# Kernel tuning notes

Hardware: AMD Instinct MI355X
Metric: run time of the kernel (lower is better)

The kernel has to match this reference:

```python
import jax, jax.numpy as jnp
import numpy as np

N = 100000   # num_labels
E = 3200000  # num edges
F_IN, H1, H2 = 384, 128, 64


def setup_inputs() -> dict:
    key = jax.random.key(0)
    k0, k1, k2, k3 = jax.random.split(key, 4)
    x = jax.random.normal(k0, (N, F_IN), dtype=jnp.float32) * 0.05
    W1 = jax.random.normal(k1, (F_IN, H1), dtype=jnp.float32) * (1.0 / np.sqrt(F_IN))
    b1 = jnp.zeros((H1,), dtype=jnp.float32)
    W2 = jax.random.normal(k2, (H1, H2), dtype=jnp.float32) * (1.0 / np.sqrt(H1))
    b2 = jnp.zeros((H2,), dtype=jnp.float32)
    edge_index = jax.random.randint(k3, (2, E), 0, N, dtype=jnp.int32)
    return {"x": x, "W1": W1, "b1": b1, "W2": W2, "b2": b2, "edge_index": edge_index}


def _gcn_norm(edge_index, num_nodes):
    # PyG gcn_norm: add self loops, deg from dst with unit weights, sym norm.
    loops = jnp.arange(num_nodes, dtype=edge_index.dtype)
    src = jnp.concatenate([edge_index[0], loops])
    dst = jnp.concatenate([edge_index[1], loops])
    deg = jax.ops.segment_sum(jnp.ones_like(dst, dtype=jnp.float32), dst,
                              num_segments=num_nodes)
    dis = jnp.where(deg > 0, jax.lax.rsqrt(deg), 0.0)
    norm = dis[src] * dis[dst]  # [E + N]
    return src, dst, norm


def _gcn_conv(x, W, b, src, dst, norm, num_nodes):
    h = x @ W                                   # [N, out]
    msg = h[src] * norm[:, None]                # gather + scale
    out = jax.ops.segment_sum(msg, dst, num_segments=num_nodes)
    return out + b


def reference(x, W1, b1, W2, b2, edge_index):
    src, dst, norm = _gcn_norm(edge_index, N)
    h = jax.nn.relu(_gcn_conv(x, W1, b1, src, dst, norm, N))
    out = _gcn_conv(h, W2, b2, src, dst, norm, N)
    return out
```

## Files before the change

kernel.cpp:

```cpp
#include <hip/hip_runtime.h>
#include <hip/hip_fp16.h>
#include <math.h>

#define N_NODES 100000
#define N_EDGES 3200000
#define F_IN    384
#define H1      128
#define H2      64

#define NBKT    782
#define HIST_W  800
#define NB_BIN  256
#define EPB     (N_EDGES / NB_BIN)

typedef _Float16 f16x8 __attribute__((ext_vector_type(8)));
typedef float    f32x4 __attribute__((ext_vector_type(4)));


__global__ __launch_bounds__(256) void k_hist(const int* __restrict__ dst,
                                              int* __restrict__ hist) {
    __shared__ int h[HIST_W];
    int b = blockIdx.x, t = threadIdx.x;
    for (int i = t; i < HIST_W; i += 256) h[i] = 0;
    __syncthreads();
    int e0 = b * EPB, e1 = e0 + EPB;
    for (int e = e0 + t; e < e1; e += 256)
        atomicAdd(&h[dst[e] >> 7], 1);
    __syncthreads();
    for (int i = t; i < HIST_W; i += 256) hist[b * HIST_W + i] = h[i];
}


__global__ __launch_bounds__(1024) void k_scan_off(int* __restrict__ hist,
                                                   int* __restrict__ bucketBase) {
    __shared__ int s[1024];
    int t = threadIdx.x;
    int run = 0;
    if (t < HIST_W) {
        #pragma unroll 8
        for (int b = 0; b < NB_BIN; b++) {
            int v = hist[b * HIST_W + t];
            hist[b * HIST_W + t] = run;
            run += v;
        }
    }
    int tot = (t < NBKT) ? run : 0;
    s[t] = tot; __syncthreads();
    for (int off = 1; off < 1024; off <<= 1) {
        int x = (t >= off) ? s[t - off] : 0;
        __syncthreads();
        s[t] += x;
        __syncthreads();
    }
    if (t <= NBKT) bucketBase[t] = s[t] - tot;
}


__global__ __launch_bounds__(256) void k_bin(const int* __restrict__ src,
                                             const int* __restrict__ dst,
                                             const int* __restrict__ hist,
                                             const int* __restrict__ bucketBase,
                                             int* __restrict__ binned) {
    __shared__ int lcur[HIST_W];
    int b = blockIdx.x, t = threadIdx.x;
    for (int i = t; i < HIST_W; i += 256)
        lcur[i] = ((i < NBKT) ? bucketBase[i] : 0) + hist[b * HIST_W + i];
    __syncthreads();
    int e0 = b * EPB, e1 = e0 + EPB;
    for (int e = e0 + t; e < e1; e += 256) {
        int d = dst[e];
        int p = atomicAdd(&lcur[d >> 7], 1);
        binned[p] = ((d & 127) << 17) | src[e];
    }
}


__global__ __launch_bounds__(256) void k_build(const int* __restrict__ binned,
                                               const int* __restrict__ bucketBase,
                                               int* __restrict__ csr,
                                               int* __restrict__ offsets,
                                               int* __restrict__ ecnt,
                                               float* __restrict__ dis) {
    __shared__ int ldeg[128], spre[128], lcur[128];
    int bkt = blockIdx.x, t = threadIdx.x;
    int e0 = bucketBase[bkt], e1 = bucketBase[bkt + 1];
    if (t < 128) ldeg[t] = 0;
    __syncthreads();
    for (int e = e0 + t; e < e1; e += 256)
        atomicAdd(&ldeg[binned[e] >> 17], 1);
    __syncthreads();
    int v = (t < 128) ? ldeg[t] : 0;
    if (t < 128) spre[t] = v;
    __syncthreads();
    for (int off = 1; off < 128; off <<= 1) {
        int x = (t < 128 && t >= off) ? spre[t - off] : 0;
        __syncthreads();
        if (t < 128) spre[t] += x;
        __syncthreads();
    }
    if (t < 128) {
        int node = bkt * 128 + t;
        if (node < N_NODES) {
            int base = e0 + spre[t] - v;
            offsets[node] = base;
            ecnt[node]    = v;
            dis[node]     = rsqrtf((float)(v + 1));
            lcur[t]       = base;
        }
    }
    __syncthreads();
    for (int e = e0 + t; e < e1; e += 256) {
        int p = binned[e];
        int pos = atomicAdd(&lcur[p >> 17], 1);
        csr[pos] = p & 0x1FFFF;
    }
}


__global__ __launch_bounds__(256) void k_w1t(const float* __restrict__ W1,
                                             __half* __restrict__ w1t) {
    int id = blockIdx.x * 256 + threadIdx.x;
    int c = id / F_IN, k = id % F_IN;
    w1t[id] = __float2half_rn(W1[(size_t)k * H1 + c]);
}


__global__ __launch_bounds__(256) void k_gemm1(const float* __restrict__ x,
                                               const __half* __restrict__ w1t,
                                               const float* __restrict__ dis,
                                               __half* __restrict__ hs1) {
    __shared__ f16x8 xl[512];
    __shared__ f16x8 wt[1024];
    int t = threadIdx.x;
    int m0 = blockIdx.x * 64;
    int wv = t >> 6, l = t & 63;
    int lrow = l & 15, kg = l >> 4;
    f32x4 acc[8];
    #pragma unroll
    for (int nb = 0; nb < 8; nb++) acc[nb] = (f32x4){0.f, 0.f, 0.f, 0.f};

    char* xb = (char*)xl;
    char* wb = (char*)wt;

    for (int k0 = 0; k0 < F_IN; k0 += 64) {
        #pragma unroll
        for (int j = 0; j < 2; j++) {
            int s = t + j * 256;
            int r = s >> 3, kc = (s & 7) * 8;
            int rg = m0 + r; if (rg >= N_NODES) rg = N_NODES - 1;
            const float* px = &x[(size_t)rg * F_IN + k0 + kc];
            float4 p0 = *(const float4*)px;
            float4 p1 = *(const float4*)(px + 4);
            f16x8 h;
            h[0] = (_Float16)p0.x; h[1] = (_Float16)p0.y;
            h[2] = (_Float16)p0.z; h[3] = (_Float16)p0.w;
            h[4] = (_Float16)p1.x; h[5] = (_Float16)p1.y;
            h[6] = (_Float16)p1.z; h[7] = (_Float16)p1.w;
            *(f16x8*)(xb + ((r * 128 + kc * 2) ^ ((r & 7) << 4))) = h;
        }
        #pragma unroll
        for (int j = 0; j < 4; j++) {
            int s = t + j * 256;
            int c = s >> 3, kc = (s & 7) * 8;
            f16x8 h = *(const f16x8*)&w1t[(size_t)c * F_IN + k0 + kc];
            *(f16x8*)(wb + ((c * 128 + kc * 2) ^ ((c & 7) << 4))) = h;
        }
        __syncthreads();
        #pragma unroll
        for (int ks = 0; ks < 2; ks++) {
            int r = wv * 16 + lrow;
            int kb = (ks * 32 + kg * 8) * 2;
            f16x8 a = *(const f16x8*)(xb + ((r * 128 + kb) ^ ((r & 7) << 4)));
            #pragma unroll
            for (int nb = 0; nb < 8; nb++) {
                int c = nb * 16 + lrow;
                f16x8 b = *(const f16x8*)(wb + ((c * 128 + kb) ^ ((c & 7) << 4)));
                acc[nb] = __builtin_amdgcn_mfma_f32_16x16x32_f16(a, b, acc[nb], 0, 0, 0);
            }
        }
        __syncthreads();
    }
    int rbase = m0 + wv * 16 + kg * 4;
    #pragma unroll
    for (int reg = 0; reg < 4; reg++) {
        int row = rbase + reg;
        if (row < N_NODES) {
            float dr = dis[row];
            #pragma unroll
            for (int nb = 0; nb < 8; nb++)
                hs1[(size_t)row * H1 + nb * 16 + lrow] = __float2half_rn(acc[nb][reg] * dr);
        }
    }
}


__global__ __launch_bounds__(256) void k_agg1(const __half* __restrict__ hs1,
                                              const float* __restrict__ dis,
                                              const int* __restrict__ csr,
                                              const int* __restrict__ offsets,
                                              const int* __restrict__ ecnt,
                                              const float* __restrict__ b1,
                                              float* __restrict__ hr) {
    int w = (blockIdx.x * 256 + threadIdx.x) >> 6;
    if (w >= N_NODES) return;
    int lane = threadIdx.x & 63;
    int j = lane * 2;
    const __half2* __restrict__ h = (const __half2*)hs1;
    float di = dis[w];
    int start = offsets[w];
    int cnt = ecnt[w];
    float2 selfv = __half22float2(h[(size_t)w * 64 + lane]);
    float sx = selfv.x;
    float sy = selfv.y;
    for (int k = 0; k < cnt; k += 8) {
        int s[8]; __half2 v[8];
        #pragma unroll
        for (int u = 0; u < 8; u++) {
            int kk = k + u;
            s[u] = csr[start + (kk < cnt ? kk : cnt - 1)];
        }
        #pragma unroll
        for (int u = 0; u < 8; u++)
            v[u] = h[(size_t)s[u] * 64 + lane];
        #pragma unroll
        for (int u = 0; u < 8; u++) {
            float2 f = __half22float2(v[u]);
            bool ok = (k + u < cnt);
            sx += ok ? f.x : 0.f;
            sy += ok ? f.y : 0.f;
        }
    }
    float2 bb = *(const float2*)&b1[j];
    float2 o = make_float2(fmaxf(bb.x + di * sx, 0.f),
                           fmaxf(bb.y + di * sy, 0.f));
    *(float2*)&hr[(size_t)w * H1 + j] = o;
}


__global__ __launch_bounds__(256) void k_gemm2(const float* __restrict__ hr,
                                               const float* __restrict__ W2,
                                               const float* __restrict__ dis,
                                               __half* __restrict__ hs2) {
    __shared__ float hl[32][128];
    __shared__ float wl[128][64];
    int t = threadIdx.x;
    int m0 = blockIdx.x * 32;
    #pragma unroll
    for (int j = 0; j < 8; j++) {
        int i4 = t + j * 256;
        int r = i4 >> 4, c4 = i4 & 15;
        *(float4*)&wl[r][c4 * 4] = *(const float4*)&W2[(size_t)r * H2 + c4 * 4];
    }
    #pragma unroll
    for (int j = 0; j < 4; j++) {
        int i4 = t + j * 256;
        int r = i4 >> 5, c4 = i4 & 31;
        *(float4*)&hl[r][c4 * 4] = *(const float4*)&hr[(size_t)(m0 + r) * H1 + c4 * 4];
    }
    __syncthreads();
    int c = t & 63, rg = t >> 6;
    float acc[8] = {};
    for (int k = 0; k < H1; k++) {
        float wv = wl[k][c];
        #pragma unroll
        for (int i = 0; i < 8; i++) acc[i] += hl[rg * 8 + i][k] * wv;
    }
    #pragma unroll
    for (int i = 0; i < 8; i++) {
        int row = m0 + rg * 8 + i;
        hs2[(size_t)row * H2 + c] = __float2half_rn(dis[row] * acc[i]);
    }
}


__global__ __launch_bounds__(256) void k_agg2(const __half* __restrict__ hs2,
                                              const float* __restrict__ dis,
                                              const int* __restrict__ csr,
                                              const int* __restrict__ offsets,
                                              const int* __restrict__ ecnt,
                                              const float* __restrict__ b2,
                                              float* __restrict__ out) {
    int w = (blockIdx.x * 256 + threadIdx.x) >> 6;
    if (w >= N_NODES) return;
    int lane = threadIdx.x & 63;
    float di = dis[w];
    int start = offsets[w];
    int cnt = ecnt[w];
    float acc = __half2float(hs2[(size_t)w * H2 + lane]);
    for (int k = 0; k < cnt; k += 8) {
        int s[8]; __half v[8];
        #pragma unroll
        for (int u = 0; u < 8; u++) {
            int kk = k + u;
            s[u] = csr[start + (kk < cnt ? kk : cnt - 1)];
        }
        #pragma unroll
        for (int u = 0; u < 8; u++)
            v[u] = hs2[(size_t)s[u] * H2 + lane];
        #pragma unroll
        for (int u = 0; u < 8; u++) {
            float f = __half2float(v[u]);
            acc += (k + u < cnt) ? f : 0.f;
        }
    }
    out[(size_t)w * H2 + lane] = b2[lane] + di * acc;
}


extern "C" void kernel_launch(void* const* d_in, const int* in_sizes, int n_in,
                              void* d_out, int out_size, void* d_ws, size_t ws_size,
                              hipStream_t stream) {
    const float* x  = (const float*)d_in[0];
    const float* W1 = (const float*)d_in[1];
    const float* b1 = (const float*)d_in[2];
    const float* W2 = (const float*)d_in[3];
    const float* b2 = (const float*)d_in[4];
    const int*   ei = (const int*)d_in[5];
    const int* src = ei;
    const int* dst = ei + N_EDGES;
    float* out = (float*)d_out;

    char* ws = (char*)d_ws;
    float* dis        = (float*)ws; ws += (size_t)N_NODES * 4;
    int*   offsets    = (int*)ws;   ws += (size_t)N_NODES * 4;
    int*   ecnt       = (int*)ws;   ws += (size_t)N_NODES * 4;
    int*   bucketBase = (int*)ws;   ws += 1024 * 4;
    int*   hist       = (int*)ws;   ws += (size_t)NB_BIN * HIST_W * 4;
    int*   csr        = (int*)ws;   ws += (size_t)N_EDGES * 4;
    __half* w1t       = (__half*)ws; ws += (size_t)H1 * F_IN * 2;
    __half* hs1       = (__half*)ws; ws += (size_t)N_NODES * H1 * 2;
    float* hr         = (float*)ws; ws += (size_t)N_NODES * H1 * 4;
    int*   binned     = (int*)hr;
    __half* hs2       = hs1;

    k_w1t     <<<(H1 * F_IN) / 256, 256, 0, stream>>>(W1, w1t);
    k_hist    <<<NB_BIN, 256, 0, stream>>>(dst, hist);
    k_scan_off<<<1, 1024, 0, stream>>>(hist, bucketBase);
    k_bin     <<<NB_BIN, 256, 0, stream>>>(src, dst, hist, bucketBase, binned);
    k_build   <<<NBKT, 256, 0, stream>>>(binned, bucketBase, csr, offsets, ecnt, dis);

    k_gemm1<<<(N_NODES + 63) / 64, 256, 0, stream>>>(x, w1t, dis, hs1);
    k_agg1<<<(N_NODES + 3) / 4, 256, 0, stream>>>(hs1, dis, csr, offsets, ecnt, b1, hr);
    k_gemm2<<<N_NODES / 32, 256, 0, stream>>>(hr, W2, dis, hs2);
    k_agg2<<<(N_NODES + 3) / 4, 256, 0, stream>>>(hs2, dis, csr, offsets, ecnt, b2, out);
}
```

Before: 634.6 us.

## Pack multiple nodes per wave in aggregation and use MFMA for second GEMM

The aggregation kernels now give each node a half-wave (layer 1) or quarter-wave (layer 2), with every lane loading 4 half-precision features as one 8-byte load. Full groups of 8 edges run without per-edge predication, and leftover edges go through a scalar tail loop. This targets underutilised lanes and narrow loads in the gather-heavy aggregation. The second GEMM is rewritten as an fp16 MFMA tile kernel with a pre-transposed fp16 W2, replacing scalar fp32 FMA. That rounds hr to fp16 before the product, which costs some precision.

```diff
diff --git a/kernel.cpp b/kernel.cpp
--- a/kernel.cpp
+++ b/kernel.cpp
@@ -122,6 +122,13 @@
     int id = blockIdx.x * 256 + threadIdx.x;
     int c = id / F_IN, k = id % F_IN;
     w1t[id] = __float2half_rn(W1[(size_t)k * H1 + c]);
+}
+
+__global__ __launch_bounds__(256) void k_w2t(const float* __restrict__ W2,
+                                             __half* __restrict__ w2t) {
+    int id = blockIdx.x * 256 + threadIdx.x;
+    int c = id / H1, k = id % H1;
+    w2t[id] = __float2half_rn(W2[(size_t)k * H2 + c]);
 }
 
 
@@ -201,74 +208,111 @@
                                               const int* __restrict__ ecnt,
                                               const float* __restrict__ b1,
                                               float* __restrict__ hr) {
-    int w = (blockIdx.x * 256 + threadIdx.x) >> 6;
-    if (w >= N_NODES) return;
-    int lane = threadIdx.x & 63;
-    int j = lane * 2;
-    const __half2* __restrict__ h = (const __half2*)hs1;
+    int t = threadIdx.x;
+    int w = blockIdx.x * 8 + ((t >> 6) << 1) + ((t & 63) >> 5);
+    int fl = t & 31;
+    int f4 = fl << 2;
     float di = dis[w];
     int start = offsets[w];
     int cnt = ecnt[w];
-    float2 selfv = __half22float2(h[(size_t)w * 64 + lane]);
-    float sx = selfv.x;
-    float sy = selfv.y;
-    for (int k = 0; k < cnt; k += 8) {
-        int s[8]; __half2 v[8];
+    uint2 selfr = *(const uint2*)(hs1 + ((unsigned)w << 7) + f4);
+    float2 s0 = __half22float2(*(__half2*)&selfr.x);
+    float2 s1 = __half22float2(*(__half2*)&selfr.y);
+    float a0 = s0.x, a1 = s0.y, a2 = s1.x, a3 = s1.y;
+
+    int kfull = cnt & ~7;
+    for (int k = 0; k < kfull; k += 8) {
+        int s[8]; uint2 r[8];
+        #pragma unroll
+        for (int u = 0; u < 8; u++) s[u] = csr[start + k + u];
+        #pragma unroll
+        for (int u = 0; u < 8; u++)
+            r[u] = *(const uint2*)(hs1 + (((unsigned)s[u] << 7) | f4));
         #pragma unroll
         for (int u = 0; u < 8; u++) {
-            int kk = k + u;
-            s[u] = csr[start + (kk < cnt ? kk : cnt - 1)];
-        }
-        #pragma unroll
-        for (int u = 0; u < 8; u++)
-            v[u] = h[(size_t)s[u] * 64 + lane];
-        #pragma unroll
-        for (int u = 0; u < 8; u++) {
-            float2 f = __half22float2(v[u]);
-            bool ok = (k + u < cnt);
-            sx += ok ? f.x : 0.f;
-            sy += ok ? f.y : 0.f;
-        }
-    }
-    float2 bb = *(const float2*)&b1[j];
-    float2 o = make_float2(fmaxf(bb.x + di * sx, 0.f),
-                           fmaxf(bb.y + di * sy, 0.f));
-    *(float2*)&hr[(size_t)w * H1 + j] = o;
+            float2 f0 = __half22float2(*(__half2*)&r[u].x);
+            float2 f1 = __half22float2(*(__half2*)&r[u].y);
+            a0 += f0.x; a1 += f0.y; a2 += f1.x; a3 += f1.y;
+        }
+    }
+    for (int k = kfull; k < cnt; k++) {
+        int s = csr[start + k];
+        uint2 rr = *(const uint2*)(hs1 + (((unsigned)s << 7) | f4));
+        float2 f0 = __half22float2(*(__half2*)&rr.x);
+        float2 f1 = __half22float2(*(__half2*)&rr.y);
+        a0 += f0.x; a1 += f0.y; a2 += f1.x; a3 += f1.y;
+    }
+    float4 bb = *(const float4*)&b1[f4];
+    float4 o = make_float4(fmaxf(bb.x + di * a0, 0.f),
+                           fmaxf(bb.y + di * a1, 0.f),
+                           fmaxf(bb.z + di * a2, 0.f),
+                           fmaxf(bb.w + di * a3, 0.f));
+    *(float4*)&hr[((size_t)w << 7) + f4] = o;
 }
 
 
 __global__ __launch_bounds__(256) void k_gemm2(const float* __restrict__ hr,
-                                               const float* __restrict__ W2,
+                                               const __half* __restrict__ w2t,
                                                const float* __restrict__ dis,
                                                __half* __restrict__ hs2) {
-    __shared__ float hl[32][128];
-    __shared__ float wl[128][64];
+    __shared__ f16x8 al[1024];
+    __shared__ f16x8 bl[1024];
     int t = threadIdx.x;
-    int m0 = blockIdx.x * 32;
-    #pragma unroll
-    for (int j = 0; j < 8; j++) {
-        int i4 = t + j * 256;
-        int r = i4 >> 4, c4 = i4 & 15;
-        *(float4*)&wl[r][c4 * 4] = *(const float4*)&W2[(size_t)r * H2 + c4 * 4];
-    }
+    int m0 = blockIdx.x * 64;
+    int wv = t >> 6, l = t & 63;
+    int lrow = l & 15, kg = l >> 4;
+    char* ab = (char*)al;
+    char* bb = (char*)bl;
+
     #pragma unroll
     for (int j = 0; j < 4; j++) {
-        int i4 = t + j * 256;
-        int r = i4 >> 5, c4 = i4 & 31;
-        *(float4*)&hl[r][c4 * 4] = *(const float4*)&hr[(size_t)(m0 + r) * H1 + c4 * 4];
-    }
-    __syncthreads();
-    int c = t & 63, rg = t >> 6;
-    float acc[8] = {};
-    for (int k = 0; k < H1; k++) {
-        float wv = wl[k][c];
-        #pragma unroll
-        for (int i = 0; i < 8; i++) acc[i] += hl[rg * 8 + i][k] * wv;
-    }
-    #pragma unroll
-    for (int i = 0; i < 8; i++) {
-        int row = m0 + rg * 8 + i;
-        hs2[(size_t)row * H2 + c] = __float2half_rn(dis[row] * acc[i]);
+        int s = t + j * 256;
+        int r = s >> 4, kc = (s & 15) * 8;
+        int rg = m0 + r; if (rg >= N_NODES) rg = N_NODES - 1;
+        const float* ph = &hr[(size_t)rg * H1 + kc];
+        float4 p0 = *(const float4*)ph;
+        float4 p1 = *(const float4*)(ph + 4);
+        f16x8 h;
+        h[0] = (_Float16)p0.x; h[1] = (_Float16)p0.y;
+        h[2] = (_Float16)p0.z; h[3] = (_Float16)p0.w;
+        h[4] = (_Float16)p1.x; h[5] = (_Float16)p1.y;
+        h[6] = (_Float16)p1.z; h[7] = (_Float16)p1.w;
+        *(f16x8*)(ab + ((r * 256 + kc * 2) ^ ((r & 7) << 4))) = h;
+    }
+    #pragma unroll
+    for (int j = 0; j < 4; j++) {
+        int s = t + j * 256;
+        int c = s >> 4, kc = (s & 15) * 8;
+        f16x8 h = *(const f16x8*)&w2t[(size_t)c * H1 + kc];
+        *(f16x8*)(bb + ((c * 256 + kc * 2) ^ ((c & 7) << 4))) = h;
+    }
+    __syncthreads();
+
+    f32x4 acc[4];
+    #pragma unroll
+    for (int nb = 0; nb < 4; nb++) acc[nb] = (f32x4){0.f, 0.f, 0.f, 0.f};
+    #pragma unroll
+    for (int ks = 0; ks < 4; ks++) {
+        int r = wv * 16 + lrow;
+        int kb = (ks * 32 + kg * 8) * 2;
+        f16x8 a = *(const f16x8*)(ab + ((r * 256 + kb) ^ ((r & 7) << 4)));
+        #pragma unroll
+        for (int nb = 0; nb < 4; nb++) {
+            int c = nb * 16 + lrow;
+            f16x8 b = *(const f16x8*)(bb + ((c * 256 + kb) ^ ((c & 7) << 4)));
+            acc[nb] = __builtin_amdgcn_mfma_f32_16x16x32_f16(a, b, acc[nb], 0, 0, 0);
+        }
+    }
+    int rbase = m0 + wv * 16 + kg * 4;
+    #pragma unroll
+    for (int reg = 0; reg < 4; reg++) {
+        int row = rbase + reg;
+        if (row < N_NODES) {
+            float dr = dis[row];
+            #pragma unroll
+            for (int nb = 0; nb < 4; nb++)
+                hs2[(size_t)row * H2 + nb * 16 + lrow] = __float2half_rn(acc[nb][reg] * dr);
+        }
     }
 }
 
@@ -280,30 +324,44 @@
                                               const int* __restrict__ ecnt,
                                               const float* __restrict__ b2,
                                               float* __restrict__ out) {
-    int w = (blockIdx.x * 256 + threadIdx.x) >> 6;
-    if (w >= N_NODES) return;
-    int lane = threadIdx.x & 63;
+    int t = threadIdx.x;
+    int w = blockIdx.x * 16 + ((t >> 6) << 2) + ((t & 63) >> 4);
+    int fl = t & 15;
+    int f4 = fl << 2;
     float di = dis[w];
     int start = offsets[w];
     int cnt = ecnt[w];
-    float acc = __half2float(hs2[(size_t)w * H2 + lane]);
-    for (int k = 0; k < cnt; k += 8) {
-        int s[8]; __half v[8];
+    uint2 selfr = *(const uint2*)(hs2 + ((unsigned)w << 6) + f4);
+    float2 s0 = __half22float2(*(__half2*)&selfr.x);
+    float2 s1 = __half22float2(*(__half2*)&selfr.y);
+    float a0 = s0.x, a1 = s0.y, a2 = s1.x, a3 = s1.y;
+
+    int kfull = cnt & ~7;
+    for (int k = 0; k < kfull; k += 8) {
+        int s[8]; uint2 r[8];
+        #pragma unroll
+        for (int u = 0; u < 8; u++) s[u] = csr[start + k + u];
+        #pragma unroll
+        for (int u = 0; u < 8; u++)
+            r[u] = *(const uint2*)(hs2 + (((unsigned)s[u] << 6) | f4));
         #pragma unroll
         for (int u = 0; u < 8; u++) {
-            int kk = k + u;
-            s[u] = csr[start + (kk < cnt ? kk : cnt - 1)];
-        }
-        #pragma unroll
-        for (int u = 0; u < 8; u++)
-            v[u] = hs2[(size_t)s[u] * H2 + lane];
-        #pragma unroll
-        for (int u = 0; u < 8; u++) {
-            float f = __half2float(v[u]);
-            acc += (k + u < cnt) ? f : 0.f;
-        }
-    }
-    out[(size_t)w * H2 + lane] = b2[lane] + di * acc;
+            float2 f0 = __half22float2(*(__half2*)&r[u].x);
+            float2 f1 = __half22float2(*(__half2*)&r[u].y);
+            a0 += f0.x; a1 += f0.y; a2 += f1.x; a3 += f1.y;
+        }
+    }
+    for (int k = kfull; k < cnt; k++) {
+        int s = csr[start + k];
+        uint2 rr = *(const uint2*)(hs2 + (((unsigned)s << 6) | f4));
+        float2 f0 = __half22float2(*(__half2*)&rr.x);
+        float2 f1 = __half22float2(*(__half2*)&rr.y);
+        a0 += f0.x; a1 += f0.y; a2 += f1.x; a3 += f1.y;
+    }
+    float4 bb = *(const float4*)&b2[f4];
+    float4 o = make_float4(bb.x + di * a0, bb.y + di * a1,
+                           bb.z + di * a2, bb.w + di * a3);
+    *(float4*)&out[((size_t)w << 6) + f4] = o;
 }
 
 
@@ -328,19 +386,21 @@
     int*   hist       = (int*)ws;   ws += (size_t)NB_BIN * HIST_W * 4;
     int*   csr        = (int*)ws;   ws += (size_t)N_EDGES * 4;
     __half* w1t       = (__half*)ws; ws += (size_t)H1 * F_IN * 2;
+    __half* w2t       = (__half*)ws; ws += (size_t)H2 * H1 * 2;
     __half* hs1       = (__half*)ws; ws += (size_t)N_NODES * H1 * 2;
     float* hr         = (float*)ws; ws += (size_t)N_NODES * H1 * 4;
     int*   binned     = (int*)hr;
     __half* hs2       = hs1;
 
     k_w1t     <<<(H1 * F_IN) / 256, 256, 0, stream>>>(W1, w1t);
+    k_w2t     <<<(H2 * H1) / 256, 256, 0, stream>>>(W2, w2t);
     k_hist    <<<NB_BIN, 256, 0, stream>>>(dst, hist);
     k_scan_off<<<1, 1024, 0, stream>>>(hist, bucketBase);
     k_bin     <<<NB_BIN, 256, 0, stream>>>(src, dst, hist, bucketBase, binned);
     k_build   <<<NBKT, 256, 0, stream>>>(binned, bucketBase, csr, offsets, ecnt, dis);
 
     k_gemm1<<<(N_NODES + 63) / 64, 256, 0, stream>>>(x, w1t, dis, hs1);
-    k_agg1<<<(N_NODES + 3) / 4, 256, 0, stream>>>(hs1, dis, csr, offsets, ecnt, b1, hr);
-    k_gemm2<<<N_NODES / 32, 256, 0, stream>>>(hr, W2, dis, hs2);
-    k_agg2<<<(N_NODES + 3) / 4, 256, 0, stream>>>(hs2, dis, csr, offsets, ecnt, b2, out);
-}
+    k_agg1<<<N_NODES / 8, 256, 0, stream>>>(hs1, dis, csr, offsets, ecnt, b1, hr);
+    k_gemm2<<<(N_NODES + 63) / 64, 256, 0, stream>>>(hr, w2t, dis, hs2);
+    k_agg2<<<N_NODES / 16, 256, 0, stream>>>(hs2, dis, csr, offsets, ecnt, b2, out);
+}
```

Result: faster. 582.8 us (-8.2%).
